# Kernel optimization log

Measured on AMD Instinct MI355X. Metric: run time of the kernel, lower is better.

The kernel has to match this reference:

```python
import jax, jax.numpy as jnp
import numpy as np

VOC, EDIM, HDIM, SSZ, SDIM, SDEPTH, NACT = 32000, 256, 256, 64, 64, 2, 3
T, B = 256, 128
PAD = 0


def setup_inputs() -> dict:
    key = jax.random.key(0)
    ks = jax.random.split(key, 20)
    s = 0.1
    inp = {
        'inputs': jax.random.randint(ks[0], (T, B), 0, VOC, dtype=jnp.int64) if jax.config.jax_enable_x64 else jax.random.randint(ks[0], (T, B), 0, VOC, dtype=jnp.int32),
        'emb_W': (jax.random.normal(ks[1], (VOC, EDIM)) * s).at[PAD].set(0.0),
        'W_hh': jax.random.normal(ks[2], (HDIM, HDIM)) * s,
        'b_hh': jnp.zeros((HDIM,)),
        'W_eh': jax.random.normal(ks[3], (HDIM, EDIM)) * s,
        'b_eh': jnp.zeros((HDIM,)),
        'W_ha': jax.random.normal(ks[4], (NACT, HDIM)) * s,
        'b_ha': jnp.zeros((NACT,)),
        'W_hg': jax.random.normal(ks[5], (1, HDIM)) * s,
        'b_hg': jnp.zeros((1,)),
        'W_hs': jax.random.normal(ks[6], (SDIM, HDIM)) * s,
        'b_hs': jnp.zeros((SDIM,)),
        'W_sh': jax.random.normal(ks[7], (HDIM, SDIM * SDEPTH)) * s,
        'b_sh': jnp.zeros((HDIM,)),
        'W_su': jax.random.normal(ks[8], (SDIM, SDIM * SDEPTH)) * s,
        'b_su': jnp.zeros((SDIM,)),
        'empty_elem': jax.random.normal(ks[9], (1, SDIM)) * s,
    }
    return inp


def _shift_down(s):  # W_down @ s : row i <- row i-1, row 0 <- 0  (push)
    return jnp.concatenate([jnp.zeros_like(s[:, :1]), s[:, :-1]], axis=1)


def _shift_up(s, k):  # (W_up)^k @ s : row i <- row i+k, tail rows <- 0 (pop)
    return jnp.concatenate([s[:, k:], jnp.zeros_like(s[:, :k])], axis=1)


def reference(inputs, emb_W, W_hh, b_hh, W_eh, b_eh, W_ha, b_ha, W_hg, b_hg,
              W_hs, b_hs, W_sh, b_sh, W_su, b_su, empty_elem):
    bsz = inputs.shape[1]
    embs = emb_W[inputs]                               # [T, B, EDIM]
    hid0 = jnp.zeros((bsz, HDIM), embs.dtype)
    stack0 = jnp.broadcast_to(empty_elem, (bsz, SSZ, SDIM))

    def step(carry, emb):
        hid, stack = carry
        tops = stack[:, :SDEPTH].reshape(bsz, SDEPTH * SDIM)
        mhid = emb @ W_eh.T + b_eh + hid @ W_hh.T + b_hh + tops @ W_sh.T + b_sh
        act_logits = hid @ W_ha.T + b_ha               # [B, 3]
        gamma = 1.0 + jax.nn.softplus(hid @ W_hg.T + b_hg)  # [B, 1]
        act = jax.nn.softmax(act_logits, axis=-1)
        sharp = act ** gamma
        sharp = sharp / (jnp.sum(sharp, axis=-1, keepdims=True) + 1e-16)
        act_chosen = jnp.argmax(sharp, axis=-1)        # topk(k=1)
        p_push = sharp[:, 0][:, None, None]
        p_pop = sharp[:, 1][:, None, None]
        p_noop = sharp[:, 2][:, None, None]
        push_val = jax.nn.relu(hid @ W_hs.T + b_hs)    # [B, SDIM]
        u_val = jax.nn.relu(tops @ W_su.T + b_su)      # [B, SDIM]
        stack_push = _shift_down(stack).at[:, 0].add(push_val)
        stack_pop = _shift_down(_shift_up(stack, SDEPTH)).at[:, 0].add(u_val)
        new_stack = p_push * stack_push + p_pop * stack_pop + p_noop * stack
        new_hid = jax.nn.relu(mhid)
        return (new_hid, new_stack), (new_hid, act_chosen)

    (hid, stack), (outputs, acts) = jax.lax.scan(step, (hid0, stack0), embs)
    return outputs, hid, stack, acts
```

## Files before the change

### kernel.cpp

```cpp
#include <hip/hip_runtime.h>

#define T_STEPS 256
#define BATCH 128

#define WEHT_OFF 0
#define WHHT_OFF 65536
#define WSHT_OFF 131072
#define WHST_OFF 163840
#define WSUT_OFF 180224
#define BC_OFF   188416

#define HID_OFF   8388608
#define STACK_OFF 8421376
#define ACTS_OFF  8945664

#define BAR_LDS() do { \
    asm volatile("s_waitcnt lgkmcnt(0)" ::: "memory"); \
    __builtin_amdgcn_s_barrier(); \
} while (0)

__global__ __launch_bounds__(256) void prep_kernel(
    const float* __restrict__ W_hh, const float* __restrict__ b_hh,
    const float* __restrict__ W_eh, const float* __restrict__ b_eh,
    const float* __restrict__ W_sh, const float* __restrict__ b_sh,
    const float* __restrict__ W_hs, const float* __restrict__ W_su,
    float* __restrict__ ws)
{
    int idx = blockIdx.x * 256 + threadIdx.x;
    if (idx < 65536) {
        ws[WEHT_OFF + idx] = W_eh[(idx & 255) * 256 + (idx >> 8)];
    } else if (idx < 131072) {
        int k = idx - 65536;
        ws[WHHT_OFF + k] = W_hh[(k & 255) * 256 + (k >> 8)];
    } else if (idx < 163840) {
        int k = idx - 131072;
        ws[WSHT_OFF + k] = W_sh[(k & 255) * 128 + (k >> 8)];
    } else if (idx < 180224) {
        int k = idx - 163840;
        ws[WHST_OFF + k] = W_hs[(k & 63) * 256 + (k >> 6)];
    } else if (idx < 188416) {
        int k = idx - 180224;
        ws[WSUT_OFF + k] = W_su[(k & 63) * 128 + (k >> 6)];
    } else if (idx < 188672) {
        int k = idx - 188416;
        ws[BC_OFF + k] = b_eh[k] + b_hh[k] + b_sh[k];
    }
}

__global__ __launch_bounds__(256) void ex_gemm(
    const int* __restrict__ tokens, const float* __restrict__ emb_W,
    const float* __restrict__ ws, float* __restrict__ outp)
{
    __shared__ __align__(16) float aT[64 * 40];
    __shared__ int tok[32];
    const int t = threadIdx.x;
    const int R0 = blockIdx.x * 32;
    if (t < 32) tok[t] = tokens[R0 + t];
    __syncthreads();

    float acc[32];
#pragma unroll
    for (int r = 0; r < 32; r++) acc[r] = 0.f;

    for (int e0 = 0; e0 < 256; e0 += 64) {
        {
            int r = t >> 3, seg = t & 7;
            const float* src = emb_W + (size_t)tok[r] * 256 + e0 + seg * 8;
            float4 v0 = *(const float4*)(src);
            float4 v1 = *(const float4*)(src + 4);
            int eb = seg * 8;
            aT[(eb + 0) * 40 + r] = v0.x; aT[(eb + 1) * 40 + r] = v0.y;
            aT[(eb + 2) * 40 + r] = v0.z; aT[(eb + 3) * 40 + r] = v0.w;
            aT[(eb + 4) * 40 + r] = v1.x; aT[(eb + 5) * 40 + r] = v1.y;
            aT[(eb + 6) * 40 + r] = v1.z; aT[(eb + 7) * 40 + r] = v1.w;
        }
        __syncthreads();
        const float* wp = ws + WEHT_OFF + (size_t)e0 * 256 + t;
#pragma unroll 4
        for (int e = 0; e < 64; e++) {
            float wv = wp[(size_t)e * 256];
            const float4* arow = (const float4*)&aT[e * 40];
#pragma unroll
            for (int j = 0; j < 8; j++) {
                float4 a4 = arow[j];
                acc[j * 4 + 0] = fmaf(a4.x, wv, acc[j * 4 + 0]);
                acc[j * 4 + 1] = fmaf(a4.y, wv, acc[j * 4 + 1]);
                acc[j * 4 + 2] = fmaf(a4.z, wv, acc[j * 4 + 2]);
                acc[j * 4 + 3] = fmaf(a4.w, wv, acc[j * 4 + 3]);
            }
        }
        __syncthreads();
    }
    float bcv = ws[BC_OFF + t];
#pragma unroll
    for (int r = 0; r < 32; r++)
        outp[(size_t)(R0 + r) * 256 + t] = acc[r] + bcv;
}

__attribute__((amdgpu_flat_work_group_size(512, 512)))
__attribute__((amdgpu_waves_per_eu(2, 2)))
__global__ void rnn_scan(
    const float* __restrict__ ws,
    const float* __restrict__ W_ha, const float* __restrict__ b_ha,
    const float* __restrict__ W_hg, const float* __restrict__ b_hg,
    const float* __restrict__ b_hs, const float* __restrict__ b_su,
    const float* __restrict__ empty_elem,
    float* __restrict__ out)
{
    __shared__ __align__(16) float hid[256];
    __shared__ __align__(16) float tops[128];
    __shared__ __align__(16) float partial[8 * 256];
    __shared__ __align__(16) float ppb[8 * 64];
    __shared__ __align__(16) float pub[8 * 64];
    __shared__ __align__(16) float bnd[16 * 64];
    __shared__ __align__(16) float wsu_l[8192];
    __shared__ __align__(16) float whs_l[16384];
    __shared__ __align__(16) float whaL[1024];
    __shared__ float scal[4];

    const int t = threadIdx.x, lane = t & 63, w = t >> 6;
    const int b = blockIdx.x;

    float4 whh[32], wsh[16];
    {
        const float* base = ws + WHHT_OFF + (size_t)(w * 32) * 256 + lane * 4;
#pragma unroll
        for (int e = 0; e < 32; e++) whh[e] = *(const float4*)(base + (size_t)e * 256);
        const float* base2 = ws + WSHT_OFF + (size_t)(w * 16) * 256 + lane * 4;
#pragma unroll
        for (int j = 0; j < 16; j++) wsh[j] = *(const float4*)(base2 + (size_t)j * 256);
    }
#pragma unroll
    for (int e = 0; e < 32; e++)
        asm volatile("" : "+v"(whh[e].x), "+v"(whh[e].y), "+v"(whh[e].z), "+v"(whh[e].w));
#pragma unroll
    for (int j = 0; j < 16; j++)
        asm volatile("" : "+v"(wsh[j].x), "+v"(wsh[j].y), "+v"(wsh[j].z), "+v"(wsh[j].w));

    float bscal = 0.f;
    if (lane == 0 && w < 4) bscal = (w < 3) ? b_ha[w] : b_hg[0];
    float bhs_r = 0.f, bsu_r = 0.f;
    if (w == 0) { bhs_r = b_hs[lane]; bsu_r = b_su[lane]; }

    const float ev = empty_elem[lane];
    float sv[8];
#pragma unroll
    for (int k = 0; k < 8; k++) sv[k] = ev;
    if (t < 256) hid[t] = 0.f;
    if (t < 128) tops[t] = empty_elem[t & 63];
    bnd[(w * 2) * 64 + lane] = ev;
    bnd[(w * 2 + 1) * 64 + lane] = ev;
    for (int i = t; i < 16384; i += 512) whs_l[i] = ws[WHST_OFF + i];
    for (int i = t; i < 8192; i += 512) {
        int j = i >> 6, s = i & 63;
        wsu_l[(j >> 2) * 256 + s * 4 + (j & 3)] = ws[WSUT_OFF + i];
    }
    for (int i = t; i < 1024; i += 512)
        whaL[i] = (i < 768) ? W_ha[i] : W_hg[i - 768];
    __syncthreads();

    float exv = (w >= 4) ? out[(size_t)b * 256 + (t - 256)] : 0.f;

    const float* whsp = &whs_l[(w * 32) * 64 + lane];

    for (int ts = 0; ts < T_STEPS; ts++) {
        float exn = 0.f;
        if (w >= 4 && ts + 1 < T_STEPS)
            exn = out[((size_t)(ts + 1) * BATCH + b) * 256 + (t - 256)];

        float halo_lo = (w == 0) ? 0.f : bnd[((w - 1) * 2 + 1) * 64 + lane];
        float halo_hi = (w == 7) ? 0.f : bnd[((w + 1) * 2) * 64 + lane];

        float4 acc = make_float4(0.f, 0.f, 0.f, 0.f);
        float accP = 0.f, accU = 0.f;
#pragma unroll
        for (int eb = 0; eb < 8; eb++) {
            float4 hv = *(const float4*)&hid[w * 32 + eb * 4];
            acc.x = fmaf(whh[eb*4+0].x, hv.x, acc.x); acc.y = fmaf(whh[eb*4+0].y, hv.x, acc.y);
            acc.z = fmaf(whh[eb*4+0].z, hv.x, acc.z); acc.w = fmaf(whh[eb*4+0].w, hv.x, acc.w);
            acc.x = fmaf(whh[eb*4+1].x, hv.y, acc.x); acc.y = fmaf(whh[eb*4+1].y, hv.y, acc.y);
            acc.z = fmaf(whh[eb*4+1].z, hv.y, acc.z); acc.w = fmaf(whh[eb*4+1].w, hv.y, acc.w);
            acc.x = fmaf(whh[eb*4+2].x, hv.z, acc.x); acc.y = fmaf(whh[eb*4+2].y, hv.z, acc.y);
            acc.z = fmaf(whh[eb*4+2].z, hv.z, acc.z); acc.w = fmaf(whh[eb*4+2].w, hv.z, acc.w);
            acc.x = fmaf(whh[eb*4+3].x, hv.w, acc.x); acc.y = fmaf(whh[eb*4+3].y, hv.w, acc.y);
            acc.z = fmaf(whh[eb*4+3].z, hv.w, acc.z); acc.w = fmaf(whh[eb*4+3].w, hv.w, acc.w);
            accP = fmaf(whsp[(eb*4+0)*64], hv.x, accP);
            accP = fmaf(whsp[(eb*4+1)*64], hv.y, accP);
            accP = fmaf(whsp[(eb*4+2)*64], hv.z, accP);
            accP = fmaf(whsp[(eb*4+3)*64], hv.w, accP);
        }
#pragma unroll
        for (int jb = 0; jb < 4; jb++) {
            float4 tv = *(const float4*)&tops[w * 16 + jb * 4];
            acc.x = fmaf(wsh[jb*4+0].x, tv.x, acc.x); acc.y = fmaf(wsh[jb*4+0].y, tv.x, acc.y);
            acc.z = fmaf(wsh[jb*4+0].z, tv.x, acc.z); acc.w = fmaf(wsh[jb*4+0].w, tv.x, acc.w);
            acc.x = fmaf(wsh[jb*4+1].x, tv.y, acc.x); acc.y = fmaf(wsh[jb*4+1].y, tv.y, acc.y);
            acc.z = fmaf(wsh[jb*4+1].z, tv.y, acc.z); acc.w = fmaf(wsh[jb*4+1].w, tv.y, acc.w);
            acc.x = fmaf(wsh[jb*4+2].x, tv.z, acc.x); acc.y = fmaf(wsh[jb*4+2].y, tv.z, acc.y);
            acc.z = fmaf(wsh[jb*4+2].z, tv.z, acc.z); acc.w = fmaf(wsh[jb*4+2].w, tv.z, acc.w);
            acc.x = fmaf(wsh[jb*4+3].x, tv.w, acc.x); acc.y = fmaf(wsh[jb*4+3].y, tv.w, acc.y);
            acc.z = fmaf(wsh[jb*4+3].z, tv.w, acc.z); acc.w = fmaf(wsh[jb*4+3].w, tv.w, acc.w);
            float4 su = *(const float4*)&wsu_l[(w * 4 + jb) * 256 + lane * 4];
            accU = fmaf(su.x, tv.x, accU);
            accU = fmaf(su.y, tv.y, accU);
            accU = fmaf(su.z, tv.z, accU);
            accU = fmaf(su.w, tv.w, accU);
        }
        *(float4*)&partial[w * 256 + lane * 4] = acc;
        ppb[w * 64 + lane] = accP;
        pub[w * 64 + lane] = accU;

        if (w < 4) {
            float bd = 0.f;
#pragma unroll
            for (int k = 0; k < 4; k++)
                bd = fmaf(whaL[w * 256 + k * 64 + lane], hid[k * 64 + lane], bd);
#pragma unroll
            for (int off = 32; off > 0; off >>= 1) bd += __shfl_down(bd, off);
            if (lane == 0) scal[w] = bd + bscal;
        }
        BAR_LDS();

        float pvv = 0.f, uvv = 0.f;
        if (w == 0) {
            float v1 = bhs_r, v2 = bsu_r;
#pragma unroll
            for (int q = 0; q < 8; q++) v1 += ppb[q * 64 + lane];
#pragma unroll
            for (int q = 0; q < 8; q++) v2 += pub[q * 64 + lane];
            pvv = fmaxf(v1, 0.f);
            uvv = fmaxf(v2, 0.f);
        }

        if (w >= 4) {
            int h = t - 256;
            float mh = exv;
#pragma unroll
            for (int q = 0; q < 8; q++) mh += partial[q * 256 + h];
            float nh = fmaxf(mh, 0.f);
            hid[h] = nh;
            out[((size_t)ts * BATCH + b) * 256 + h] = nh;
        }

        float l0 = scal[0], l1 = scal[1], l2 = scal[2], gv = scal[3];
        float eg = __expf(gv);
        float g = 1.f + ((gv > 15.f) ? gv : __logf(1.f + eg));
        float m = fmaxf(l0, fmaxf(l1, l2));
        float z = __expf(l0 - m) + __expf(l1 - m) + __expf(l2 - m);
        float lz = __logf(z);
        float s0  = __expf(g * (l0 - m - lz));
        float s1v = __expf(g * (l1 - m - lz));
        float s2v = __expf(g * (l2 - m - lz));
        float S = s0 + s1v + s2v + 1e-16f;
        float rS = __builtin_amdgcn_rcpf(S);
        float p0 = s0 * rS, p1 = s1v * rS, p2 = s2v * rS;

        if (t == 0) {
            int am = 0; float bm = s0;
            if (s1v > bm) { bm = s1v; am = 1; }
            if (s2v > bm) { bm = s2v; am = 2; }
            out[ACTS_OFF + ts * BATCH + b] = (float)am;
        }

        {
            float nv[8];
            float below0 = (w == 0) ? pvv : halo_lo;
            float pop0   = (w == 0) ? uvv : sv[1];
            nv[0] = fmaf(p0, below0, fmaf(p1, pop0, p2 * sv[0]));
#pragma unroll
            for (int k = 1; k < 7; k++)
                nv[k] = fmaf(p0, sv[k - 1], fmaf(p1, sv[k + 1], p2 * sv[k]));
            nv[7] = fmaf(p0, sv[6], fmaf(p1, halo_hi, p2 * sv[7]));
#pragma unroll
            for (int k = 0; k < 8; k++) sv[k] = nv[k];
        }
        bnd[(w * 2) * 64 + lane] = sv[0];
        bnd[(w * 2 + 1) * 64 + lane] = sv[7];
        if (w == 0) { tops[lane] = sv[0]; tops[64 + lane] = sv[1]; }

        exv = exn;
        BAR_LDS();
    }

    if (t < 256) out[HID_OFF + (size_t)b * 256 + t] = hid[t];
#pragma unroll
    for (int k = 0; k < 8; k++)
        out[STACK_OFF + (size_t)b * 4096 + (w * 8 + k) * 64 + lane] = sv[k];
}

extern "C" void kernel_launch(void* const* d_in, const int* in_sizes, int n_in,
                              void* d_out, int out_size, void* d_ws, size_t ws_size,
                              hipStream_t stream)
{
    (void)in_sizes; (void)n_in; (void)out_size; (void)ws_size;
    const int*   inputs     = (const int*)d_in[0];
    const float* emb_W      = (const float*)d_in[1];
    const float* W_hh       = (const float*)d_in[2];
    const float* b_hh       = (const float*)d_in[3];
    const float* W_eh       = (const float*)d_in[4];
    const float* b_eh       = (const float*)d_in[5];
    const float* W_ha       = (const float*)d_in[6];
    const float* b_ha       = (const float*)d_in[7];
    const float* W_hg       = (const float*)d_in[8];
    const float* b_hg       = (const float*)d_in[9];
    const float* W_hs       = (const float*)d_in[10];
    const float* b_hs       = (const float*)d_in[11];
    const float* W_sh       = (const float*)d_in[12];
    const float* b_sh       = (const float*)d_in[13];
    const float* W_su       = (const float*)d_in[14];
    const float* b_su       = (const float*)d_in[15];
    const float* empty_elem = (const float*)d_in[16];
    float* out = (float*)d_out;
    float* ws  = (float*)d_ws;

    hipLaunchKernelGGL(prep_kernel, dim3(737), dim3(256), 0, stream,
                       W_hh, b_hh, W_eh, b_eh, W_sh, b_sh, W_hs, W_su, ws);
    hipLaunchKernelGGL(ex_gemm, dim3(1024), dim3(256), 0, stream,
                       inputs, emb_W, ws, out);
    hipLaunchKernelGGL(rnn_scan, dim3(128), dim3(512), 0, stream,
                       ws, W_ha, b_ha, W_hg, b_hg, b_hs, b_su, empty_elem, out);
}
```

Before: 689.1 us.

## Keep W_hs/W_su slices in registers and broadcast hid/tops via readlane

Moves each wave's W_hs and W_su weight slices from LDS into VGPRs, adding 48 registers per thread. It then loads one hid/tops element per lane once per step and broadcasts it with v_readlane instead of repeated LDS float4 loads. The aim is to remove per-step LDS traffic and latency from the recurrent inner loop and shrink LDS usage. The cost is higher register pressure at the fixed 2-waves-per-EU budget, which risks spills, and each readlane puts a scalar-to-vector dependency into the FMA chain.

```diff
diff --git a/kernel.cpp b/kernel.cpp
--- a/kernel.cpp
+++ b/kernel.cpp
@@ -18,6 +18,10 @@
     asm volatile("s_waitcnt lgkmcnt(0)" ::: "memory"); \
     __builtin_amdgcn_s_barrier(); \
 } while (0)
+
+__device__ __forceinline__ float rl(float v, int l) {
+    return __int_as_float(__builtin_amdgcn_readlane(__float_as_int(v), l));
+}
 
 __global__ __launch_bounds__(256) void prep_kernel(
     const float* __restrict__ W_hh, const float* __restrict__ b_hh,
@@ -113,8 +117,6 @@
     __shared__ __align__(16) float ppb[8 * 64];
     __shared__ __align__(16) float pub[8 * 64];
     __shared__ __align__(16) float bnd[16 * 64];
-    __shared__ __align__(16) float wsu_l[8192];
-    __shared__ __align__(16) float whs_l[16384];
     __shared__ __align__(16) float whaL[1024];
     __shared__ float scal[4];
 
@@ -122,6 +124,7 @@
     const int b = blockIdx.x;
 
     float4 whh[32], wsh[16];
+    float  whs_r[32], wsu_r[16];
     {
         const float* base = ws + WHHT_OFF + (size_t)(w * 32) * 256 + lane * 4;
 #pragma unroll
@@ -129,6 +132,12 @@
         const float* base2 = ws + WSHT_OFF + (size_t)(w * 16) * 256 + lane * 4;
 #pragma unroll
         for (int j = 0; j < 16; j++) wsh[j] = *(const float4*)(base2 + (size_t)j * 256);
+        const float* base3 = ws + WHST_OFF + (size_t)(w * 32) * 64 + lane;
+#pragma unroll
+        for (int e = 0; e < 32; e++) whs_r[e] = base3[(size_t)e * 64];
+        const float* base4 = ws + WSUT_OFF + (size_t)(w * 16) * 64 + lane;
+#pragma unroll
+        for (int j = 0; j < 16; j++) wsu_r[j] = base4[(size_t)j * 64];
     }
 #pragma unroll
     for (int e = 0; e < 32; e++)
@@ -136,6 +145,12 @@
 #pragma unroll
     for (int j = 0; j < 16; j++)
         asm volatile("" : "+v"(wsh[j].x), "+v"(wsh[j].y), "+v"(wsh[j].z), "+v"(wsh[j].w));
+#pragma unroll
+    for (int e = 0; e < 32; e += 4)
+        asm volatile("" : "+v"(whs_r[e]), "+v"(whs_r[e+1]), "+v"(whs_r[e+2]), "+v"(whs_r[e+3]));
+#pragma unroll
+    for (int j = 0; j < 16; j += 4)
+        asm volatile("" : "+v"(wsu_r[j]), "+v"(wsu_r[j+1]), "+v"(wsu_r[j+2]), "+v"(wsu_r[j+3]));
 
     float bscal = 0.f;
     if (lane == 0 && w < 4) bscal = (w < 3) ? b_ha[w] : b_hg[0];
@@ -150,18 +165,14 @@
     if (t < 128) tops[t] = empty_elem[t & 63];
     bnd[(w * 2) * 64 + lane] = ev;
     bnd[(w * 2 + 1) * 64 + lane] = ev;
-    for (int i = t; i < 16384; i += 512) whs_l[i] = ws[WHST_OFF + i];
-    for (int i = t; i < 8192; i += 512) {
-        int j = i >> 6, s = i & 63;
-        wsu_l[(j >> 2) * 256 + s * 4 + (j & 3)] = ws[WSUT_OFF + i];
-    }
     for (int i = t; i < 1024; i += 512)
         whaL[i] = (i < 768) ? W_ha[i] : W_hg[i - 768];
     __syncthreads();
 
+    const float* slice_ptr = (lane < 32) ? &hid[w * 32 + lane]
+                                         : &tops[w * 16 + (lane & 15)];
+
     float exv = (w >= 4) ? out[(size_t)b * 256 + (t - 256)] : 0.f;
-
-    const float* whsp = &whs_l[(w * 32) * 64 + lane];
 
     for (int ts = 0; ts < T_STEPS; ts++) {
         float exn = 0.f;
@@ -171,40 +182,26 @@
         float halo_lo = (w == 0) ? 0.f : bnd[((w - 1) * 2 + 1) * 64 + lane];
         float halo_hi = (w == 7) ? 0.f : bnd[((w + 1) * 2) * 64 + lane];
 
+        float slice = *slice_ptr;
         float4 acc = make_float4(0.f, 0.f, 0.f, 0.f);
         float accP = 0.f, accU = 0.f;
 #pragma unroll
-        for (int eb = 0; eb < 8; eb++) {
-            float4 hv = *(const float4*)&hid[w * 32 + eb * 4];
-            acc.x = fmaf(whh[eb*4+0].x, hv.x, acc.x); acc.y = fmaf(whh[eb*4+0].y, hv.x, acc.y);
-            acc.z = fmaf(whh[eb*4+0].z, hv.x, acc.z); acc.w = fmaf(whh[eb*4+0].w, hv.x, acc.w);
-            acc.x = fmaf(whh[eb*4+1].x, hv.y, acc.x); acc.y = fmaf(whh[eb*4+1].y, hv.y, acc.y);
-            acc.z = fmaf(whh[eb*4+1].z, hv.y, acc.z); acc.w = fmaf(whh[eb*4+1].w, hv.y, acc.w);
-            acc.x = fmaf(whh[eb*4+2].x, hv.z, acc.x); acc.y = fmaf(whh[eb*4+2].y, hv.z, acc.y);
-            acc.z = fmaf(whh[eb*4+2].z, hv.z, acc.z); acc.w = fmaf(whh[eb*4+2].w, hv.z, acc.w);
-            acc.x = fmaf(whh[eb*4+3].x, hv.w, acc.x); acc.y = fmaf(whh[eb*4+3].y, hv.w, acc.y);
-            acc.z = fmaf(whh[eb*4+3].z, hv.w, acc.z); acc.w = fmaf(whh[eb*4+3].w, hv.w, acc.w);
-            accP = fmaf(whsp[(eb*4+0)*64], hv.x, accP);
-            accP = fmaf(whsp[(eb*4+1)*64], hv.y, accP);
-            accP = fmaf(whsp[(eb*4+2)*64], hv.z, accP);
-            accP = fmaf(whsp[(eb*4+3)*64], hv.w, accP);
-        }
-#pragma unroll
-        for (int jb = 0; jb < 4; jb++) {
-            float4 tv = *(const float4*)&tops[w * 16 + jb * 4];
-            acc.x = fmaf(wsh[jb*4+0].x, tv.x, acc.x); acc.y = fmaf(wsh[jb*4+0].y, tv.x, acc.y);
-            acc.z = fmaf(wsh[jb*4+0].z, tv.x, acc.z); acc.w = fmaf(wsh[jb*4+0].w, tv.x, acc.w);
-            acc.x = fmaf(wsh[jb*4+1].x, tv.y, acc.x); acc.y = fmaf(wsh[jb*4+1].y, tv.y, acc.y);
-            acc.z = fmaf(wsh[jb*4+1].z, tv.y, acc.z); acc.w = fmaf(wsh[jb*4+1].w, tv.y, acc.w);
-            acc.x = fmaf(wsh[jb*4+2].x, tv.z, acc.x); acc.y = fmaf(wsh[jb*4+2].y, tv.z, acc.y);
-            acc.z = fmaf(wsh[jb*4+2].z, tv.z, acc.z); acc.w = fmaf(wsh[jb*4+2].w, tv.z, acc.w);
-            acc.x = fmaf(wsh[jb*4+3].x, tv.w, acc.x); acc.y = fmaf(wsh[jb*4+3].y, tv.w, acc.y);
-            acc.z = fmaf(wsh[jb*4+3].z, tv.w, acc.z); acc.w = fmaf(wsh[jb*4+3].w, tv.w, acc.w);
-            float4 su = *(const float4*)&wsu_l[(w * 4 + jb) * 256 + lane * 4];
-            accU = fmaf(su.x, tv.x, accU);
-            accU = fmaf(su.y, tv.y, accU);
-            accU = fmaf(su.z, tv.z, accU);
-            accU = fmaf(su.w, tv.w, accU);
+        for (int e = 0; e < 32; e++) {
+            float hv = rl(slice, e);
+            acc.x = fmaf(whh[e].x, hv, acc.x);
+            acc.y = fmaf(whh[e].y, hv, acc.y);
+            acc.z = fmaf(whh[e].z, hv, acc.z);
+            acc.w = fmaf(whh[e].w, hv, acc.w);
+            accP  = fmaf(whs_r[e], hv, accP);
+        }
+#pragma unroll
+        for (int j = 0; j < 16; j++) {
+            float tv = rl(slice, 32 + j);
+            acc.x = fmaf(wsh[j].x, tv, acc.x);
+            acc.y = fmaf(wsh[j].y, tv, acc.y);
+            acc.z = fmaf(wsh[j].z, tv, acc.z);
+            acc.w = fmaf(wsh[j].w, tv, acc.w);
+            accU  = fmaf(wsu_r[j], tv, accU);
         }
         *(float4*)&partial[w * 256 + lane * 4] = acc;
         ppb[w * 64 + lane] = accP;
```

Result: slower. 1.276 ms (+85.2%).
